# Optimization experiments

Hardware: AMD Instinct MI355X
Metric: run time of the kernel (lower is better)

The kernel has to match this reference:

```python
import jax, jax.numpy as jnp
import numpy as np


def setup_inputs() -> dict:
    key = jax.random.key(0)
    k1, k2, k3, k4 = jax.random.split(key, 4)
    num_out_groups, num_in_groups = 8192, 1024
    num_codebooks, codebook_size, out_group_size, in_group_size = 2, 65536, 1, 8
    codes = jax.random.randint(k1, (num_out_groups, num_in_groups, num_codebooks), 0, codebook_size, dtype=jnp.int32)
    codebooks = jax.random.normal(k2, (num_codebooks, codebook_size, out_group_size, in_group_size), dtype=jnp.float32)
    scales = jax.random.uniform(k3, (num_out_groups, num_in_groups, 1, 1), dtype=jnp.float32)
    zeros = jax.random.normal(k4, (num_out_groups, num_in_groups, 1, 1), dtype=jnp.float32)
    return {"codes": codes, "codebooks": codebooks, "scales": scales, "zeros": zeros}


def reference(codes, codebooks, scales, zeros):
    # codes: [no, ni, nc] int; codebooks: [nc, cs, og, ig]
    # scales/zeros: broadcastable with [no, ni, og, ig]
    nc, cs, og, ig = codebooks.shape
    no, ni, _ = codes.shape
    # gather-sum across codebooks (embedding_bag mode='sum' equivalent)
    # gathered: [no, ni, nc, og, ig]
    gathered = codebooks[jnp.arange(nc)[None, None, :], codes]
    w = gathered.sum(axis=2)  # [no, ni, og, ig]
    w = w * scales + zeros
    # swap (ni, og) then merge groups -> [no*og, ni*ig]
    return w.swapaxes(1, 2).reshape(no * og, ni * ig)
```

## Files before the change

kernel.cpp:

```cpp
#include <hip/hip_runtime.h>


typedef float    vf4 __attribute__((ext_vector_type(4)));
typedef int      vi4 __attribute__((ext_vector_type(4)));
typedef int      vi2 __attribute__((ext_vector_type(2)));
typedef _Float16 vh2 __attribute__((ext_vector_type(2)));
typedef _Float16 vh8 __attribute__((ext_vector_type(8)));

__global__ __launch_bounds__(256) void
repack_kernel(const float* __restrict__ cbs, _Float16* __restrict__ cb16)
{
    const int i = blockIdx.x * blockDim.x + threadIdx.x;
    const vf4* in4 = (const vf4*)cbs;
    vf4 a = in4[2 * i];
    vf4 b = in4[2 * i + 1];
    vh8 h;
    h[0] = (_Float16)a.x; h[1] = (_Float16)a.y;
    h[2] = (_Float16)a.z; h[3] = (_Float16)a.w;
    h[4] = (_Float16)b.x; h[5] = (_Float16)b.y;
    h[6] = (_Float16)b.z; h[7] = (_Float16)b.w;
    *(vh8*)(cb16 + (size_t)8 * i) = h;
}

__global__ __launch_bounds__(256, 4) void
dequant_fp16(const int* __restrict__ codes,
             const _Float16* __restrict__ cb16,
             const float* __restrict__ cbs,
             const float* __restrict__ scales,
             const float* __restrict__ zeros,
             float* __restrict__ out,
             int total)
{
    __shared__ __align__(16) char lds_raw[4 * 4096];
    const int lane = threadIdx.x & 63;
    const int wid  = threadIdx.x >> 6;
    char* wlds = lds_raw + wid * 4096;

    const int  nwaves = (gridDim.x * blockDim.x) >> 6;
    const int  wave   = (blockIdx.x * blockDim.x + threadIdx.x) >> 6;
    const long wstep  = (long)nwaves * 256;

    const vi4* codes4 = (const vi4*)codes;

    const int half = lane & 1;
    const int hoff = half * 4;
    const int pidx = lane >> 1;

    const float* szsrc = (lane < 32) ? scales : zeros;
    const int    sl    = lane & 31;
    char* szdst = wlds + 2048 + ((lane >> 5) << 10) + (sl << 4);

    long gbase = (long)wave * 256;

    if (gbase + 256 <= total) {
        vi4 pc0  = __builtin_nontemporal_load(codes4 + (gbase >> 1) + lane);
        vi4 pc1  = __builtin_nontemporal_load(codes4 + (gbase >> 1) + 64 + lane);
        vf4 psz0 = __builtin_nontemporal_load((const vf4*)(szsrc + gbase) + sl);
        vf4 psz1 = __builtin_nontemporal_load((const vf4*)(szsrc + gbase) + 32 + sl);

        for (;;) {
            const long gcur = gbase;
            gbase += wstep;
            const bool more = (gbase + 256 <= total);

            *(vi4*)(wlds + lane * 16)        = pc0;
            *(vi4*)(wlds + 1024 + lane * 16) = pc1;
            *(vf4*)szdst                     = psz0;
            *(vf4*)(szdst + 512)             = psz1;

            if (more) {
                pc0  = __builtin_nontemporal_load(codes4 + (gbase >> 1) + lane);
                pc1  = __builtin_nontemporal_load(codes4 + (gbase >> 1) + 64 + lane);
                psz0 = __builtin_nontemporal_load((const vf4*)(szsrc + gbase) + sl);
                psz1 = __builtin_nontemporal_load((const vf4*)(szsrc + gbase) + 32 + sl);
            }

            vi2 c0 = *(const vi2*)(wlds + (0 * 32 + pidx) * 8);
            vi2 c1 = *(const vi2*)(wlds + (1 * 32 + pidx) * 8);
            vi2 c2 = *(const vi2*)(wlds + (2 * 32 + pidx) * 8);
            vi2 c3 = *(const vi2*)(wlds + (3 * 32 + pidx) * 8);
            vi2 c4 = *(const vi2*)(wlds + (4 * 32 + pidx) * 8);
            vi2 c5 = *(const vi2*)(wlds + (5 * 32 + pidx) * 8);
            vi2 c6 = *(const vi2*)(wlds + (6 * 32 + pidx) * 8);
            vi2 c7 = *(const vi2*)(wlds + (7 * 32 + pidx) * 8);

            const int k0 = half ? (c0.y | 65536) : c0.x;
            const int k1 = half ? (c1.y | 65536) : c1.x;
            const int k2 = half ? (c2.y | 65536) : c2.x;
            const int k3 = half ? (c3.y | 65536) : c3.x;
            const int k4 = half ? (c4.y | 65536) : c4.x;
            const int k5 = half ? (c5.y | 65536) : c5.x;
            const int k6 = half ? (c6.y | 65536) : c6.x;
            const int k7 = half ? (c7.y | 65536) : c7.x;
            vi4 e0 = *(const vi4*)(cb16 + ((size_t)(unsigned)k0 << 3));
            vi4 e1 = *(const vi4*)(cb16 + ((size_t)(unsigned)k1 << 3));
            vi4 e2 = *(const vi4*)(cb16 + ((size_t)(unsigned)k2 << 3));
            vi4 e3 = *(const vi4*)(cb16 + ((size_t)(unsigned)k3 << 3));
            vi4 e4 = *(const vi4*)(cb16 + ((size_t)(unsigned)k4 << 3));
            vi4 e5 = *(const vi4*)(cb16 + ((size_t)(unsigned)k5 << 3));
            vi4 e6 = *(const vi4*)(cb16 + ((size_t)(unsigned)k6 << 3));
            vi4 e7 = *(const vi4*)(cb16 + ((size_t)(unsigned)k7 << 3));

            float* ob = out + (size_t)gcur * 8 + pidx * 8 + hoff;

            #pragma unroll
            for (int k = 0; k < 8; ++k) {
                vi4 e = (k == 0) ? e0 : (k == 1) ? e1 : (k == 2) ? e2 :
                        (k == 3) ? e3 : (k == 4) ? e4 : (k == 5) ? e5 :
                        (k == 6) ? e6 : e7;
                int send0 = half ? e.x : e.z;
                int send1 = half ? e.y : e.w;
                int own0  = half ? e.z : e.x;
                int own1  = half ? e.w : e.y;
                int recv0 = __shfl_xor(send0, 1);
                int recv1 = __shfl_xor(send1, 1);
                vh2 s0 = __builtin_bit_cast(vh2, own0) + __builtin_bit_cast(vh2, recv0);
                vh2 s1 = __builtin_bit_cast(vh2, own1) + __builtin_bit_cast(vh2, recv1);

                float s = *(const float*)(wlds + 2048 + (k * 32 + pidx) * 4);
                float z = *(const float*)(wlds + 3072 + (k * 32 + pidx) * 4);
                vf4 r;
                r.x = (float)s0.x * s + z;
                r.y = (float)s0.y * s + z;
                r.z = (float)s1.x * s + z;
                r.w = (float)s1.y * s + z;
                __builtin_nontemporal_store(r, (vf4*)(ob + k * 256));
            }
            if (!more) break;
        }
    }

    const size_t CB1 = (size_t)65536 * 8;
    const long total_full = ((long)total >> 8) << 8;
    const int  gtid  = blockIdx.x * blockDim.x + threadIdx.x;
    const long pstep = (long)(gridDim.x * blockDim.x) >> 1;
    for (long g = total_full + (gtid >> 1); g < total; g += pstep) {
        vi2  c = *(const vi2*)(codes + (size_t)2 * g);
        float s = scales[g];
        float z = zeros[g];
        vf4 a0 = *(const vf4*)(cbs + ((size_t)c.x << 3) + hoff);
        vf4 a1 = *(const vf4*)(cbs + CB1 + ((size_t)c.y << 3) + hoff);
        vf4 r  = (a0 + a1) * s + z;
        __builtin_nontemporal_store(r, (vf4*)(out + (size_t)g * 8 + hoff));
    }
}

__global__ __launch_bounds__(256) void
dequant_f32(const int* __restrict__ codes,
            const float* __restrict__ cbs,
            const float* __restrict__ scales,
            const float* __restrict__ zeros,
            float* __restrict__ out,
            int total)
{
    const size_t CB1 = (size_t)65536 * 8;
    const vi2* codes2 = (const vi2*)codes;
    const int tid   = blockIdx.x * blockDim.x + threadIdx.x;
    const int half  = tid & 1;
    const int hoff  = half * 4;
    const int gstep = (gridDim.x * blockDim.x) >> 1;
    for (int g = tid >> 1; g < total; g += gstep) {
        vi2  c = __builtin_nontemporal_load(codes2 + g);
        float s = __builtin_nontemporal_load(scales + g);
        float z = __builtin_nontemporal_load(zeros + g);
        vf4 e0 = *(const vf4*)(cbs + ((size_t)c.x << 3) + hoff);
        vf4 e1 = *(const vf4*)(cbs + CB1 + ((size_t)c.y << 3) + hoff);
        vf4 r  = (e0 + e1) * s + z;
        __builtin_nontemporal_store(r, (vf4*)(out + (size_t)g * 8 + hoff));
    }
}

extern "C" void kernel_launch(void* const* d_in, const int* in_sizes, int n_in,
                              void* d_out, int out_size, void* d_ws, size_t ws_size,
                              hipStream_t stream) {
    const int*   codes     = (const int*)  d_in[0];
    const float* codebooks = (const float*)d_in[1];
    const float* scales    = (const float*)d_in[2];
    const float* zeros     = (const float*)d_in[3];
    float*       out       = (float*)d_out;

    const int total = in_sizes[0] / 2;
    const size_t cb16_bytes = (size_t)2 * 65536 * 8 * sizeof(_Float16);

    if (ws_size >= cb16_bytes) {
        _Float16* cb16 = (_Float16*)d_ws;
        repack_kernel<<<512, 256, 0, stream>>>(codebooks, cb16);
        dequant_fp16<<<2048, 256, 0, stream>>>(
            codes, cb16, codebooks, scales, zeros, out, total);
    } else {
        dequant_f32<<<2048, 256, 0, stream>>>(
            codes, codebooks, scales, zeros, out, total);
    }
}
```

Baseline: 133.5 us.

## Software-pipeline codebook gathers with double-buffered LDS staging

Result: slower. 141.0 us (+5.6%).

```diff
diff --git a/kernel.cpp b/kernel.cpp
--- a/kernel.cpp
+++ b/kernel.cpp
@@ -22,6 +22,89 @@
     *(vh8*)(cb16 + (size_t)8 * i) = h;
 }
 
+struct GSet { vi4 e0, e1, e2, e3, e4, e5, e6, e7; };
+
+__device__ __forceinline__ void
+load_stream(const vi4* codes4, const float* szsrc, int lane, int sl, long gb,
+            vi4& pc0, vi4& pc1, vf4& psz0, vf4& psz1)
+{
+    pc0  = __builtin_nontemporal_load(codes4 + (gb >> 1) + lane);
+    pc1  = __builtin_nontemporal_load(codes4 + (gb >> 1) + 64 + lane);
+    psz0 = __builtin_nontemporal_load((const vf4*)(szsrc + gb) + sl);
+    psz1 = __builtin_nontemporal_load((const vf4*)(szsrc + gb) + 32 + sl);
+}
+
+__device__ __forceinline__ void
+stage(char* buf, int lane, int szoff, vi4 pc0, vi4 pc1, vf4 psz0, vf4 psz1)
+{
+    *(vi4*)(buf + lane * 16)        = pc0;
+    *(vi4*)(buf + 1024 + lane * 16) = pc1;
+    *(vf4*)(buf + szoff)            = psz0;
+    *(vf4*)(buf + szoff + 512)      = psz1;
+}
+
+__device__ __forceinline__ vi4
+gload(const _Float16* cb16, int k)
+{
+    return *(const vi4*)(cb16 + ((size_t)(unsigned)k << 3));
+}
+
+__device__ __forceinline__ void
+issue_gathers(const char* buf, int half, int pidx, const _Float16* cb16, GSet& g)
+{
+    vi2 c0 = *(const vi2*)(buf + (0 * 32 + pidx) * 8);
+    vi2 c1 = *(const vi2*)(buf + (1 * 32 + pidx) * 8);
+    vi2 c2 = *(const vi2*)(buf + (2 * 32 + pidx) * 8);
+    vi2 c3 = *(const vi2*)(buf + (3 * 32 + pidx) * 8);
+    vi2 c4 = *(const vi2*)(buf + (4 * 32 + pidx) * 8);
+    vi2 c5 = *(const vi2*)(buf + (5 * 32 + pidx) * 8);
+    vi2 c6 = *(const vi2*)(buf + (6 * 32 + pidx) * 8);
+    vi2 c7 = *(const vi2*)(buf + (7 * 32 + pidx) * 8);
+    g.e0 = gload(cb16, half ? (c0.y | 65536) : c0.x);
+    g.e1 = gload(cb16, half ? (c1.y | 65536) : c1.x);
+    g.e2 = gload(cb16, half ? (c2.y | 65536) : c2.x);
+    g.e3 = gload(cb16, half ? (c3.y | 65536) : c3.x);
+    g.e4 = gload(cb16, half ? (c4.y | 65536) : c4.x);
+    g.e5 = gload(cb16, half ? (c5.y | 65536) : c5.x);
+    g.e6 = gload(cb16, half ? (c6.y | 65536) : c6.x);
+    g.e7 = gload(cb16, half ? (c7.y | 65536) : c7.x);
+}
+
+__device__ __forceinline__ void
+consume_one(vi4 e, const char* buf, int k, int half, int pidx, float* ob)
+{
+    int send0 = half ? e.x : e.z;
+    int send1 = half ? e.y : e.w;
+    int own0  = half ? e.z : e.x;
+    int own1  = half ? e.w : e.y;
+    int recv0 = __shfl_xor(send0, 1);
+    int recv1 = __shfl_xor(send1, 1);
+    vh2 s0 = __builtin_bit_cast(vh2, own0) + __builtin_bit_cast(vh2, recv0);
+    vh2 s1 = __builtin_bit_cast(vh2, own1) + __builtin_bit_cast(vh2, recv1);
+
+    float s = *(const float*)(buf + 2048 + (k * 32 + pidx) * 4);
+    float z = *(const float*)(buf + 3072 + (k * 32 + pidx) * 4);
+    vf4 r;
+    r.x = (float)s0.x * s + z;
+    r.y = (float)s0.y * s + z;
+    r.z = (float)s1.x * s + z;
+    r.w = (float)s1.y * s + z;
+    __builtin_nontemporal_store(r, (vf4*)(ob + k * 256));
+}
+
+__device__ __forceinline__ void
+consume_all(const GSet& g, const char* buf, int half, int pidx, float* ob)
+{
+    consume_one(g.e0, buf, 0, half, pidx, ob);
+    consume_one(g.e1, buf, 1, half, pidx, ob);
+    consume_one(g.e2, buf, 2, half, pidx, ob);
+    consume_one(g.e3, buf, 3, half, pidx, ob);
+    consume_one(g.e4, buf, 4, half, pidx, ob);
+    consume_one(g.e5, buf, 5, half, pidx, ob);
+    consume_one(g.e6, buf, 6, half, pidx, ob);
+    consume_one(g.e7, buf, 7, half, pidx, ob);
+}
+
 __global__ __launch_bounds__(256, 4) void
 dequant_fp16(const int* __restrict__ codes,
              const _Float16* __restrict__ cb16,
@@ -31,102 +114,62 @@
              float* __restrict__ out,
              int total)
 {
-    __shared__ __align__(16) char lds_raw[4 * 4096];
+    __shared__ __align__(16) char lds_raw[4 * 8192];
     const int lane = threadIdx.x & 63;
     const int wid  = threadIdx.x >> 6;
-    char* wlds = lds_raw + wid * 4096;
+    char* buf0 = lds_raw + wid * 8192;
+    char* buf1 = buf0 + 4096;
 
     const int  nwaves = (gridDim.x * blockDim.x) >> 6;
     const int  wave   = (blockIdx.x * blockDim.x + threadIdx.x) >> 6;
     const long wstep  = (long)nwaves * 256;
 
     const vi4* codes4 = (const vi4*)codes;
-
     const int half = lane & 1;
     const int hoff = half * 4;
     const int pidx = lane >> 1;
 
     const float* szsrc = (lane < 32) ? scales : zeros;
     const int    sl    = lane & 31;
-    char* szdst = wlds + 2048 + ((lane >> 5) << 10) + (sl << 4);
-
-    long gbase = (long)wave * 256;
-
-    if (gbase + 256 <= total) {
-        vi4 pc0  = __builtin_nontemporal_load(codes4 + (gbase >> 1) + lane);
-        vi4 pc1  = __builtin_nontemporal_load(codes4 + (gbase >> 1) + 64 + lane);
-        vf4 psz0 = __builtin_nontemporal_load((const vf4*)(szsrc + gbase) + sl);
-        vf4 psz1 = __builtin_nontemporal_load((const vf4*)(szsrc + gbase) + 32 + sl);
-
-        for (;;) {
-            const long gcur = gbase;
-            gbase += wstep;
-            const bool more = (gbase + 256 <= total);
-
-            *(vi4*)(wlds + lane * 16)        = pc0;
-            *(vi4*)(wlds + 1024 + lane * 16) = pc1;
-            *(vf4*)szdst                     = psz0;
-            *(vf4*)(szdst + 512)             = psz1;
-
-            if (more) {
-                pc0  = __builtin_nontemporal_load(codes4 + (gbase >> 1) + lane);
-                pc1  = __builtin_nontemporal_load(codes4 + (gbase >> 1) + 64 + lane);
-                psz0 = __builtin_nontemporal_load((const vf4*)(szsrc + gbase) + sl);
-                psz1 = __builtin_nontemporal_load((const vf4*)(szsrc + gbase) + 32 + sl);
+    const int    szoff = 2048 + ((lane >> 5) << 10) + (sl << 4);
+
+    const long base = (long)wave * 256;
+    long nit = 0;
+    if (base + 256 <= total) nit = (total - base - 256) / wstep + 1;
+
+    if (nit > 0) {
+        vi4 pc0, pc1; vf4 psz0, psz1;
+        GSet A, B;
+
+        load_stream(codes4, szsrc, lane, sl, base, pc0, pc1, psz0, psz1);
+        stage(buf0, lane, szoff, pc0, pc1, psz0, psz1);
+        if (nit > 1)
+            load_stream(codes4, szsrc, lane, sl, base + wstep, pc0, pc1, psz0, psz1);
+        issue_gathers(buf0, half, pidx, cb16, A);
+
+        long t = 0;
+        for (; t + 2 <= nit; t += 2) {
+            stage(buf1, lane, szoff, pc0, pc1, psz0, psz1);
+            if (t + 2 < nit)
+                load_stream(codes4, szsrc, lane, sl, base + (t + 2) * wstep,
+                            pc0, pc1, psz0, psz1);
+            issue_gathers(buf1, half, pidx, cb16, B);
+            consume_all(A, buf0, half, pidx,
+                        out + (size_t)(base + t * wstep) * 8 + pidx * 8 + hoff);
+
+            if (t + 2 < nit) {
+                stage(buf0, lane, szoff, pc0, pc1, psz0, psz1);
+                if (t + 3 < nit)
+                    load_stream(codes4, szsrc, lane, sl, base + (t + 3) * wstep,
+                                pc0, pc1, psz0, psz1);
+                issue_gathers(buf0, half, pidx, cb16, A);
             }
-
-            vi2 c0 = *(const vi2*)(wlds + (0 * 32 + pidx) * 8);
-            vi2 c1 = *(const vi2*)(wlds + (1 * 32 + pidx) * 8);
-            vi2 c2 = *(const vi2*)(wlds + (2 * 32 + pidx) * 8);
-            vi2 c3 = *(const vi2*)(wlds + (3 * 32 + pidx) * 8);
-            vi2 c4 = *(const vi2*)(wlds + (4 * 32 + pidx) * 8);
-            vi2 c5 = *(const vi2*)(wlds + (5 * 32 + pidx) * 8);
-            vi2 c6 = *(const vi2*)(wlds + (6 * 32 + pidx) * 8);
-            vi2 c7 = *(const vi2*)(wlds + (7 * 32 + pidx) * 8);
-
-            const int k0 = half ? (c0.y | 65536) : c0.x;
-            const int k1 = half ? (c1.y | 65536) : c1.x;
-            const int k2 = half ? (c2.y | 65536) : c2.x;
-            const int k3 = half ? (c3.y | 65536) : c3.x;
-            const int k4 = half ? (c4.y | 65536) : c4.x;
-            const int k5 = half ? (c5.y | 65536) : c5.x;
-            const int k6 = half ? (c6.y | 65536) : c6.x;
-            const int k7 = half ? (c7.y | 65536) : c7.x;
-            vi4 e0 = *(const vi4*)(cb16 + ((size_t)(unsigned)k0 << 3));
-            vi4 e1 = *(const vi4*)(cb16 + ((size_t)(unsigned)k1 << 3));
-            vi4 e2 = *(const vi4*)(cb16 + ((size_t)(unsigned)k2 << 3));
-            vi4 e3 = *(const vi4*)(cb16 + ((size_t)(unsigned)k3 << 3));
-            vi4 e4 = *(const vi4*)(cb16 + ((size_t)(unsigned)k4 << 3));
-            vi4 e5 = *(const vi4*)(cb16 + ((size_t)(unsigned)k5 << 3));
-            vi4 e6 = *(const vi4*)(cb16 + ((size_t)(unsigned)k6 << 3));
-            vi4 e7 = *(const vi4*)(cb16 + ((size_t)(unsigned)k7 << 3));
-
-            float* ob = out + (size_t)gcur * 8 + pidx * 8 + hoff;
-
-            #pragma unroll
-            for (int k = 0; k < 8; ++k) {
-                vi4 e = (k == 0) ? e0 : (k == 1) ? e1 : (k == 2) ? e2 :
-                        (k == 3) ? e3 : (k == 4) ? e4 : (k == 5) ? e5 :
-                        (k == 6) ? e6 : e7;
-                int send0 = half ? e.x : e.z;
-                int send1 = half ? e.y : e.w;
-                int own0  = half ? e.z : e.x;
-                int own1  = half ? e.w : e.y;
-                int recv0 = __shfl_xor(send0, 1);
-                int recv1 = __shfl_xor(send1, 1);
-                vh2 s0 = __builtin_bit_cast(vh2, own0) + __builtin_bit_cast(vh2, recv0);
-                vh2 s1 = __builtin_bit_cast(vh2, own1) + __builtin_bit_cast(vh2, recv1);
-
-                float s = *(const float*)(wlds + 2048 + (k * 32 + pidx) * 4);
-                float z = *(const float*)(wlds + 3072 + (k * 32 + pidx) * 4);
-                vf4 r;
-                r.x = (float)s0.x * s + z;
-                r.y = (float)s0.y * s + z;
-                r.z = (float)s1.x * s + z;
-                r.w = (float)s1.y * s + z;
-                __builtin_nontemporal_store(r, (vf4*)(ob + k * 256));
-            }
-            if (!more) break;
+            consume_all(B, buf1, half, pidx,
+                        out + (size_t)(base + (t + 1) * wstep) * 8 + pidx * 8 + hoff);
+        }
+        if (t < nit) {
+            consume_all(A, buf0, half, pidx,
+                        out + (size_t)(base + t * wstep) * 8 + pidx * 8 + hoff);
         }
     }
 
```
